# Optimization experiments

Measured on AMD Instinct MI355X. Metric: run time of the kernel, lower is better.

The kernel has to match this reference:

```python
import jax, jax.numpy as jnp
import numpy as np
import math

B, TQ, TK, D = 4, 1024, 1024, 1024
H, DK, DV = 16, 64, 64


def _ln(x, g, b, eps=1e-5):
    m = x.mean(-1, keepdims=True)
    v = ((x - m) ** 2).mean(-1, keepdims=True)
    return (x - m) * jax.lax.rsqrt(v + eps) * g + b


def setup_inputs() -> dict:
    key = jax.random.key(0)
    ks = jax.random.split(key, 24)
    s = 0.02
    inp = {
        "x": jax.random.normal(ks[0], (B, TQ, D), jnp.float32),
        "y": jax.random.normal(ks[1], (B, TK, D), jnp.float32),
        "mask": jax.random.randint(ks[2], (B, TK), 0, 2).astype(bool),
        # pre-attention layernorms (affine)
        "ln1_g": jnp.ones((D,)), "ln1_b": jnp.zeros((D,)),
        "ln2_g": jnp.ones((D,)), "ln2_b": jnp.zeros((D,)),
        # mha1 projections
        "q_w": jax.random.normal(ks[3], (D, H * DK)) * s, "q_b": jnp.zeros((H * DK,)),
        "k_w": jax.random.normal(ks[4], (D, H * DK)) * s, "k_b": jnp.zeros((H * DK,)),
        "v_w": jax.random.normal(ks[5], (D, H * DV)) * s, "v_b": jnp.zeros((H * DV,)),
        "o_w": jax.random.normal(ks[6], (H * DV, D)) * s, "o_b": jnp.zeros((D,)),
        # MLP: [LN, ReLU, Linear] x 2 over sizes [D, D, D]
        "mln1_g": jnp.ones((D,)), "mln1_b": jnp.zeros((D,)),
        "l1_w": jax.random.normal(ks[7], (D, D)) * s, "l1_b": jnp.zeros((D,)),
        "mln2_g": jnp.ones((D,)), "mln2_b": jnp.zeros((D,)),
        "l2_w": jax.random.normal(ks[8], (D, D)) * s, "l2_b": jnp.zeros((D,)),
    }
    return inp


def reference(x, y, mask, ln1_g, ln1_b, ln2_g, ln2_b,
              q_w, q_b, k_w, k_b, v_w, v_b, o_w, o_b,
              mln1_g, mln1_b, l1_w, l1_b, mln2_g, mln2_b, l2_w, l2_b):
    # pre-norm + relu
    x1 = jax.nn.relu(_ln(x, ln1_g, ln1_b))
    y1 = jax.nn.relu(_ln(y, ln2_g, ln2_b))
    # cross attention (mha1)
    b, t, _ = x1.shape
    q = (x1 @ q_w + q_b).reshape(b, t, H, DK)
    k = (y1 @ k_w + k_b).reshape(b, -1, H, DK)
    v = (y1 @ v_w + v_b).reshape(b, -1, H, DV)
    logits = jnp.einsum('bthd,bThd->bhtT', q, k) * (1.0 / math.sqrt(DK))
    logits = jnp.where(mask[:, None, None, :], logits, -1e30)
    w = jax.nn.softmax(logits, axis=-1)
    attn = jnp.einsum('bhtT,bThd->bthd', w, v).reshape(b, t, H * DV)
    x = x + (attn @ o_w + o_b)
    # MLP: LN -> ReLU -> Linear, twice
    h = jax.nn.relu(_ln(x, mln1_g, mln1_b)) @ l1_w + l1_b
    out = jax.nn.relu(_ln(h, mln2_g, mln2_b)) @ l2_w + l2_b
    return out
```

## Files before the change

### kernel.cpp

```cpp
#include <hip/hip_runtime.h>
#include <hip/hip_bf16.h>
#include <math.h>

#define D_MODEL 1024
#define NTOK    4096

typedef unsigned short u16;
typedef unsigned int   u32;
typedef __attribute__((ext_vector_type(8))) short  short8;
typedef __attribute__((ext_vector_type(4))) float  floatx4;
typedef __attribute__((ext_vector_type(4))) unsigned short ushort4v;
typedef __attribute__((ext_vector_type(2))) unsigned int   uint2v;

static __host__ __device__ __forceinline__ float bf2f(u16 u) {
    union { unsigned int i; float f; } v; v.i = ((unsigned int)u) << 16; return v.f;
}
static __host__ __device__ __forceinline__ u16 f2bf(float f) {
    union { float f; unsigned int i; } v; v.f = f;
    unsigned int r = (v.i + 0x7FFFu + ((v.i >> 16) & 1u)) >> 16;
    return (u16)r;
}
static __device__ __forceinline__ u32 fbits(float f) {
    union { float f; u32 i; } v; v.f = f; return v.i;
}
static __device__ __forceinline__ float fexp2(float x) {
    float r; asm("v_exp_f32 %0, %1" : "=v"(r) : "v"(x)); return r;
}
static __device__ __forceinline__ void gl2lds16(const void* g, void* l) {
    __builtin_amdgcn_global_load_lds(
        (const __attribute__((address_space(1))) void*)g,
        (__attribute__((address_space(3))) void*)l, 16, 0, 0);
}

__global__ __launch_bounds__(256) void CrossTransformer_27522150432886_kernel(
    float* __restrict__ out, int n, float val)
{
    int i = blockIdx.x * 256 + threadIdx.x;
    if (i < n) out[i] = val;
}

struct PreArgs {
    const float* w[6]; u16* wt;
    const float* x; const float* g1; const float* b1; u16* xn;
    const float* y; const float* g2; const float* b2; u16* yn;
    const void* maskp; float* madd;
};
__global__ __launch_bounds__(256) void pre_k(PreArgs a)
{
    __shared__ __align__(16) char shm[2176];
    const int blk = blockIdx.x, t = threadIdx.x;

    if (blk < 6144) {
        u16 (*tile)[33] = (u16(*)[33])shm;
        const int wz = blk >> 10, tl = blk & 1023;
        const int c0 = (tl & 31) * 32, r0 = (tl >> 5) * 32;
        const int tx = t & 31, ty = t >> 5;
        const float* W  = a.w[wz];
        u16*         Wt = a.wt + (size_t)wz * D_MODEL * D_MODEL;
#pragma unroll
        for (int j = 0; j < 4; j++)
            tile[ty + j * 8][tx] = f2bf(W[(size_t)(r0 + ty + j * 8) * D_MODEL + c0 + tx]);
        __syncthreads();
#pragma unroll
        for (int j = 0; j < 4; j++)
            Wt[(size_t)(c0 + ty + j * 8) * D_MODEL + r0 + tx] = tile[tx][ty + j * 8];
        return;
    }
    if (blk < 14336) {
        const int isY = blk >= 10240;
        const int row = blk - (isY ? 10240 : 6144);
        const float* in  = isY ? a.y  : a.x;
        const float* gam = isY ? a.g2 : a.g1;
        const float* bet = isY ? a.b2 : a.b1;
        u16*         out = isY ? a.yn : a.xn;
        float (*red)[4] = (float(*)[4])shm;

        const float4 p = *(const float4*)(in + (size_t)row * D_MODEL + t * 4);
        float v0 = p.x, v1 = p.y, v2 = p.z, v3 = p.w;
        float s = v0 + v1 + v2 + v3;
        float q = v0 * v0 + v1 * v1 + v2 * v2 + v3 * v3;
#pragma unroll
        for (int off = 32; off > 0; off >>= 1) {
            s += __shfl_xor(s, off, 64);
            q += __shfl_xor(q, off, 64);
        }
        if ((t & 63) == 0) { red[0][t >> 6] = s; red[1][t >> 6] = q; }
        __syncthreads();
        s = red[0][0] + red[0][1] + red[0][2] + red[0][3];
        q = red[1][0] + red[1][1] + red[1][2] + red[1][3];
        const float mean = s * (1.0f / D_MODEL);
        const float var  = q * (1.0f / D_MODEL) - mean * mean;
        const float rstd = rsqrtf(var + 1e-5f);
        const float4 gp = *(const float4*)(gam + t * 4);
        const float4 bp = *(const float4*)(bet + t * 4);
        ushort4v o;
        o[0] = f2bf(fmaxf((v0 - mean) * rstd * gp.x + bp.x, 0.f));
        o[1] = f2bf(fmaxf((v1 - mean) * rstd * gp.y + bp.y, 0.f));
        o[2] = f2bf(fmaxf((v2 - mean) * rstd * gp.z + bp.z, 0.f));
        o[3] = f2bf(fmaxf((v3 - mean) * rstd * gp.w + bp.w, 0.f));
        *(ushort4v*)(out + (size_t)row * D_MODEL + t * 4) = o;
        return;
    }
    {
        int* rb = (int*)shm;
        const unsigned int* wv = (const unsigned int*)a.maskp;
        int bad = 0;
        for (int i = t; i < 1024; i += 256) {
            unsigned int v = wv[i];
            if (!(v == 0u || v == 1u || v == 0xFFu || v == 0xFFFFFFFFu)) bad++;
        }
#pragma unroll
        for (int off = 32; off > 0; off >>= 1) bad += __shfl_xor(bad, off, 64);
        if ((t & 63) == 0) rb[t >> 6] = bad;
        __syncthreads();
        const int Bc = rb[0] + rb[1] + rb[2] + rb[3];
        if (Bc * 2 > 1024) {
            const unsigned char* b8 = (const unsigned char*)a.maskp;
            for (int i = t; i < 4096; i += 256) a.madd[i] = b8[i] ? 0.f : -1e30f;
        } else {
            const int* m32 = (const int*)a.maskp;
            for (int i = t; i < 4096; i += 256) a.madd[i] = m32[i] ? 0.f : -1e30f;
        }
    }
}

__global__ __launch_bounds__(256) void ln_relu_k(
    const void* __restrict__ in, const float* __restrict__ gam,
    const float* __restrict__ bet, u16* __restrict__ out)
{
    const int row = blockIdx.x, t = threadIdx.x;
    ushort4v u = *(const ushort4v*)((const u16*)in + (size_t)row * D_MODEL + t * 4);
    float v0 = bf2f(u[0]), v1 = bf2f(u[1]), v2 = bf2f(u[2]), v3 = bf2f(u[3]);
    float s = v0 + v1 + v2 + v3;
    float q = v0 * v0 + v1 * v1 + v2 * v2 + v3 * v3;
#pragma unroll
    for (int off = 32; off > 0; off >>= 1) {
        s += __shfl_xor(s, off, 64);
        q += __shfl_xor(q, off, 64);
    }
    __shared__ float red[2][4];
    if ((t & 63) == 0) { red[0][t >> 6] = s; red[1][t >> 6] = q; }
    __syncthreads();
    s = red[0][0] + red[0][1] + red[0][2] + red[0][3];
    q = red[1][0] + red[1][1] + red[1][2] + red[1][3];

    const float mean = s * (1.0f / D_MODEL);
    const float var  = q * (1.0f / D_MODEL) - mean * mean;
    const float rstd = rsqrtf(var + 1e-5f);

    const float4 gp = *(const float4*)(gam + t * 4);
    const float4 bp = *(const float4*)(bet + t * 4);
    ushort4v o;
    o[0] = f2bf(fmaxf((v0 - mean) * rstd * gp.x + bp.x, 0.f));
    o[1] = f2bf(fmaxf((v1 - mean) * rstd * gp.y + bp.y, 0.f));
    o[2] = f2bf(fmaxf((v2 - mean) * rstd * gp.z + bp.z, 0.f));
    o[3] = f2bf(fmaxf((v3 - mean) * rstd * gp.w + bp.w, 0.f));
    *(ushort4v*)(out + (size_t)row * D_MODEL + t * 4) = o;
}

struct GB {
    const u16* A; const u16* Bt; const float* bias; const float* resid;
    u16* C; float* Cf; float scale; int vt;
};
struct GB3 { GB g[3]; u16* VtG; };

__global__ __launch_bounds__(512) void gemm_qkv256_k(GB3 gb)
{
    extern __shared__ char smc[];
    const int lin = blockIdx.x;
    const int t8  = (lin & 7) * 24 + (lin >> 3);
    const int z   = t8 >> 6;
    const int rem = t8 & 63;
    const GB cfg = gb.g[z];
    const int t = threadIdx.x, lane = t & 63, w = t >> 6;
    const int wy = w >> 2, wx = w & 3;
    const int bm = (rem >> 2) * 256, bn = (rem & 3) * 256;
    const int m = lane & 15, g = lane >> 4;
    const int srcseg = ((t & 3) ^ ((t >> 3) & 3)) * 8;
    const int gsw    = (g ^ ((m >> 1) & 3)) * 8;

    const u16* Ag = cfg.A  + (size_t)(bm + (t >> 2)) * D_MODEL + srcseg;
    const u16* Bg = cfg.Bt + (size_t)(bn + (t >> 2)) * D_MODEL + srcseg;

    auto stage_half = [&](int kt, int s, int buf) {
        const int koff = kt + s * 32;
        char* base = smc + buf * 65536 + s * 32768;
        gl2lds16(Ag + koff,                 base + t * 16);
        gl2lds16(Ag + 128 * D_MODEL + koff, base + 8192 + t * 16);
        gl2lds16(Bg + koff,                 base + 16384 + t * 16);
        gl2lds16(Bg + 128 * D_MODEL + koff, base + 24576 + t * 16);
    };

    floatx4 acc[8][4] = {};
    const int NT = D_MODEL / 64;

    stage_half(0, 0, 0);
    stage_half(0, 1, 0);

    int buf = 0;
    for (int tt = 0; tt < NT; ++tt) {
        const int ktn = ((tt + 1) & (NT - 1)) * 64;
        const int nbuf = buf ^ 1;
#pragma unroll
        for (int s = 0; s < 2; ++s) {
            asm volatile("s_waitcnt vmcnt(4)" ::: "memory");
            __builtin_amdgcn_s_barrier();
            stage_half(ktn, s, nbuf);

            const u16* As = (const u16*)(smc + buf * 65536 + s * 32768);
            const u16* Bs = As + 8192;
            short8 af[8], bf[4];
#pragma unroll
            for (int mt = 0; mt < 8; mt++)
                af[mt] = *(const short8*)(As + (wy * 128 + mt * 16 + m) * 32 + gsw);
#pragma unroll
            for (int nt = 0; nt < 4; nt++)
                bf[nt] = *(const short8*)(Bs + (wx * 64 + nt * 16 + m) * 32 + gsw);

            __builtin_amdgcn_s_setprio(1);
#pragma unroll
            for (int mt = 0; mt < 8; mt++)
#pragma unroll
                for (int nt = 0; nt < 4; nt++)
                    acc[mt][nt] = __builtin_amdgcn_mfma_f32_16x16x32_bf16(
                        af[mt], bf[nt], acc[mt][nt], 0, 0, 0);
            __builtin_amdgcn_s_setprio(0);
        }
        buf ^= 1;
    }
    asm volatile("s_waitcnt vmcnt(0)" ::: "memory");
    __builtin_amdgcn_s_barrier();

    float bv[4];
#pragma unroll
    for (int nt = 0; nt < 4; nt++)
        bv[nt] = cfg.bias[bn + wx * 64 + nt * 16 + m];

    if (!cfg.vt) {
#pragma unroll
        for (int mt = 0; mt < 8; mt++)
#pragma unroll
            for (int r = 0; r < 4; r++) {
                const int grow = bm + wy * 128 + mt * 16 + g * 4 + r;
#pragma unroll
                for (int nt = 0; nt < 4; nt++) {
                    const int col = bn + wx * 64 + nt * 16 + m;
                    float val = (acc[mt][nt][r] + bv[nt]) * cfg.scale;
                    cfg.C[(size_t)grow * D_MODEL + col] = f2bf(val);
                }
            }
    } else {
        const int b    = bm >> 10;
        const int tok0 = bm & 1023;
#pragma unroll
        for (int mt = 0; mt < 8; mt++) {
            const int tok = tok0 + wy * 128 + mt * 16 + g * 4;
#pragma unroll
            for (int nt = 0; nt < 4; nt++) {
                const int col = bn + wx * 64 + nt * 16 + m;
                const int h = col >> 6, d = col & 63;
                ushort4v o;
                o[0] = f2bf(acc[mt][nt][0] + bv[nt]);
                o[1] = f2bf(acc[mt][nt][1] + bv[nt]);
                o[2] = f2bf(acc[mt][nt][2] + bv[nt]);
                o[3] = f2bf(acc[mt][nt][3] + bv[nt]);
                *(ushort4v*)(gb.VtG + ((size_t)((b * 16 + h) * 64 + d)) * 1024 + tok) = o;
            }
        }
    }
}

__global__ __launch_bounds__(512) void gemm_out_k(GB cfg)
{
    const int lin = blockIdx.x + 8 * blockIdx.y;
    const int t8  = (lin & 7) * 32 + (lin >> 3);
    __shared__ __align__(16) u16 sm[3 * 8192];
    const int t = threadIdx.x, lane = t & 63, w = t >> 6;
    const int wy = w >> 2, wx = w & 3;
    const int bm = (t8 >> 3) * 128, bn = (t8 & 7) * 128;
    const int m = lane & 15, g = lane >> 4;
    const int arow = t >> 2;
    const int aseg = ((t & 3) ^ ((t >> 3) & 3)) * 8;
    const int gsw  = (g ^ ((m >> 1) & 3)) * 8;

    const u16* Ag = cfg.A  + (size_t)(bm + arow) * D_MODEL + aseg;
    const u16* Bg = cfg.Bt + (size_t)(bn + arow) * D_MODEL + aseg;

    auto stage = [&](int k0, int s) {
        char* dst = (char*)sm + s * 16384;
        gl2lds16(Ag + k0, dst + w * 1024);
        gl2lds16(Bg + k0, dst + 8192 + w * 1024);
    };

    floatx4 acc[4][2] = {};
    const int NT = D_MODEL / 32;

    stage(0, 0);
    stage(32, 1);
    asm volatile("s_waitcnt vmcnt(2)" ::: "memory");
    __builtin_amdgcn_s_barrier();

    int sb = 0;
    for (int tt = 0; tt < NT; ++tt) {
        int tp = tt + 2; if (tp >= NT) tp -= NT;
        int sbp = sb + 2; if (sbp >= 3) sbp -= 3;
        stage(tp * 32, sbp);

        const u16* As = sm + sb * 8192;
        const u16* Bs = As + 4096;
        short8 af[4], bf[2];
#pragma unroll
        for (int mt = 0; mt < 4; mt++)
            af[mt] = *(const short8*)(As + (wy * 64 + mt * 16 + m) * 32 + gsw);
#pragma unroll
        for (int nt = 0; nt < 2; nt++)
            bf[nt] = *(const short8*)(Bs + (wx * 32 + nt * 16 + m) * 32 + gsw);

        __builtin_amdgcn_s_setprio(1);
#pragma unroll
        for (int mt = 0; mt < 4; mt++)
#pragma unroll
            for (int nt = 0; nt < 2; nt++)
                acc[mt][nt] = __builtin_amdgcn_mfma_f32_16x16x32_bf16(
                    af[mt], bf[nt], acc[mt][nt], 0, 0, 0);
        __builtin_amdgcn_s_setprio(0);

        asm volatile("s_waitcnt vmcnt(2)" ::: "memory");
        __builtin_amdgcn_s_barrier();
        sb = sb + 1; if (sb >= 3) sb -= 3;
    }
    asm volatile("s_waitcnt vmcnt(0)" ::: "memory");

    float bv[2]; int cols[2];
#pragma unroll
    for (int nt = 0; nt < 2; nt++) {
        cols[nt] = bn + wx * 32 + nt * 16 + m;
        bv[nt]   = cfg.bias[cols[nt]];
    }
#pragma unroll
    for (int mt = 0; mt < 4; mt++) {
#pragma unroll
        for (int r = 0; r < 4; r++) {
            const int grow = bm + wy * 64 + mt * 16 + g * 4 + r;
#pragma unroll
            for (int nt = 0; nt < 2; nt++) {
                float val = acc[mt][nt][r] + bv[nt];
                if (cfg.resid) val += cfg.resid[(size_t)grow * D_MODEL + cols[nt]];
                if (cfg.Cf) cfg.Cf[(size_t)grow * D_MODEL + cols[nt]] = val;
                else        cfg.C [(size_t)grow * D_MODEL + cols[nt]] = f2bf(val);
            }
        }
    }
}

__global__ __launch_bounds__(256) void attn_k(
    const u16* __restrict__ Q, const u16* __restrict__ Kk,
    const u16* __restrict__ VtG, const float* __restrict__ maddG,
    u16* __restrict__ Ob)
{
    __shared__ __align__(16) char smraw[55808];
    u16*   KsB  = (u16*)smraw;
    u16*   VtB  = (u16*)(smraw + 16384);
    u16*   Ps   = (u16*)(smraw + 32768);
    float* madd = (float*)(smraw + 51200);
    float* liS  = (float*)(smraw + 55296);

    const int lin = blockIdx.x + 8 * (blockIdx.y + 16 * blockIdx.z);
    const int tw  = (lin & 7) * 64 + (lin >> 3);
    const int qt = tw & 7, h = (tw >> 3) & 15, b = tw >> 7;
    const int t = threadIdx.x, lane = t & 63, w = t >> 6;
    const int m = lane & 15, g = lane >> 4;

    for (int i = t; i < 1024; i += 256) madd[i] = maddG[b * 1024 + i];

    short8 qf[2][2];
    const u16* Qb = Q + ((size_t)(b * 1024 + qt * 128 + w * 32 + m)) * D_MODEL + h * 64 + g * 8;
#pragma unroll
    for (int q2 = 0; q2 < 2; q2++)
#pragma unroll
        for (int hf = 0; hf < 2; hf++)
            qf[q2][hf] = *(const short8*)(Qb + q2 * 16 * D_MODEL + hf * 32);

    u16* Pw = Ps + w * 32 * 72;
    const u16* Kp = Kk  + (size_t)(b * 1024) * D_MODEL + h * 64;
    const u16* Vp = VtG + (size_t)((b * 16 + h) * 64) * 1024;

    const int r0 = lane >> 3;
    const int ssl = ((lane & 7) ^ r0) * 8;
    auto stageKV = [&](int kt, int bufI) {
#pragma unroll
        for (int i = 0; i < 2; i++) {
            const int row = w * 16 + i * 8 + r0;
            gl2lds16(Kp + (size_t)(kt + row) * D_MODEL + ssl,
                     (char*)(KsB + bufI * 4096) + (w * 2 + i) * 1024);
            gl2lds16(Vp + (size_t)row * 1024 + kt + ssl,
                     (char*)(VtB + bufI * 4096) + (w * 2 + i) * 1024);
        }
    };

    floatx4 Ov[2][4] = {};
    float li[2] = { 0.f, 0.f };

    const int s8  = m & 7;
    const int sl0 = (g ^ s8) * 8;
    const int sl1 = sl0 ^ 32;

    stageKV(0, 0);
    __syncthreads();

    int buf = 0;
    for (int kt = 0; kt < 1024; kt += 64) {
        if (kt + 64 < 1024) stageKV(kt + 64, buf ^ 1);

        const u16* Ks = KsB + buf * 4096;
        const u16* Vt = VtB + buf * 4096;

        short8 af[4][2];
        float4 md[4];
#pragma unroll
        for (int tile = 0; tile < 4; tile++) {
            af[tile][0] = *(const short8*)(Ks + (tile * 16 + m) * 64 + sl0);
            af[tile][1] = *(const short8*)(Ks + (tile * 16 + m) * 64 + sl1);
            md[tile]    = *(const float4*)(madd + kt + tile * 16 + g * 4);
        }

#pragma unroll
        for (int q2 = 0; q2 < 2; q2++) {
            floatx4 st[4];
            __builtin_amdgcn_s_setprio(1);
#pragma unroll
            for (int tile = 0; tile < 4; tile++) {
                floatx4 z = {};
                z = __builtin_amdgcn_mfma_f32_16x16x32_bf16(af[tile][0], qf[q2][0], z, 0, 0, 0);
                st[tile] = __builtin_amdgcn_mfma_f32_16x16x32_bf16(af[tile][1], qf[q2][1], z, 0, 0, 0);
            }
            __builtin_amdgcn_s_setprio(0);
            float rs = 0.f;
#pragma unroll
            for (int tile = 0; tile < 4; tile++) {
                float p0 = fexp2(st[tile][0] + md[tile].x);
                float p1 = fexp2(st[tile][1] + md[tile].y);
                float p2 = fexp2(st[tile][2] + md[tile].z);
                float p3 = fexp2(st[tile][3] + md[tile].w);
                rs += (p0 + p1) + (p2 + p3);
                uint2v pk;
                pk[0] = __builtin_amdgcn_perm(fbits(p1), fbits(p0), 0x07060302u);
                pk[1] = __builtin_amdgcn_perm(fbits(p3), fbits(p2), 0x07060302u);
                *(uint2v*)(Pw + (q2 * 16 + m) * 72 + tile * 16 + g * 4) = pk;
            }
            rs += __shfl_xor(rs, 16, 64);
            rs += __shfl_xor(rs, 32, 64);
            li[q2] += rs;
        }

        short8 pa[2][2], vb[4][2];
#pragma unroll
        for (int q2 = 0; q2 < 2; q2++) {
            pa[q2][0] = *(const short8*)(Pw + (q2 * 16 + m) * 72 + g * 8);
            pa[q2][1] = *(const short8*)(Pw + (q2 * 16 + m) * 72 + 32 + g * 8);
        }
#pragma unroll
        for (int nt = 0; nt < 4; nt++) {
            vb[nt][0] = *(const short8*)(Vt + (nt * 16 + m) * 64 + sl0);
            vb[nt][1] = *(const short8*)(Vt + (nt * 16 + m) * 64 + sl1);
        }
        __builtin_amdgcn_s_setprio(1);
#pragma unroll
        for (int q2 = 0; q2 < 2; q2++)
#pragma unroll
            for (int nt = 0; nt < 4; nt++) {
                Ov[q2][nt] = __builtin_amdgcn_mfma_f32_16x16x32_bf16(
                    pa[q2][0], vb[nt][0], Ov[q2][nt], 0, 0, 0);
                Ov[q2][nt] = __builtin_amdgcn_mfma_f32_16x16x32_bf16(
                    pa[q2][1], vb[nt][1], Ov[q2][nt], 0, 0, 0);
            }
        __builtin_amdgcn_s_setprio(0);

        asm volatile("s_waitcnt vmcnt(0)" ::: "memory");
        __builtin_amdgcn_s_barrier();
        buf ^= 1;
    }

    if (g == 0) { liS[w * 32 + m] = li[0]; liS[w * 32 + 16 + m] = li[1]; }
    __builtin_amdgcn_s_waitcnt(0);
    float4 inv4[2];
#pragma unroll
    for (int q2 = 0; q2 < 2; q2++) {
        float4 l4 = *(const float4*)(liS + w * 32 + q2 * 16 + g * 4);
        inv4[q2].x = 1.0f / fmaxf(l4.x, 1e-37f);
        inv4[q2].y = 1.0f / fmaxf(l4.y, 1e-37f);
        inv4[q2].z = 1.0f / fmaxf(l4.z, 1e-37f);
        inv4[q2].w = 1.0f / fmaxf(l4.w, 1e-37f);
    }
#pragma unroll
    for (int q2 = 0; q2 < 2; q2++) {
        const float iv[4] = { inv4[q2].x, inv4[q2].y, inv4[q2].z, inv4[q2].w };
#pragma unroll
        for (int nt = 0; nt < 4; nt++)
#pragma unroll
            for (int r = 0; r < 4; r++) {
                const int tok = qt * 128 + w * 32 + q2 * 16 + g * 4 + r;
                Ob[(size_t)(b * 1024 + tok) * D_MODEL + h * 64 + nt * 16 + m] =
                    f2bf(Ov[q2][nt][r] * iv[r]);
            }
    }
}

extern "C" __attribute__((visibility("default")))
void kernel_launch(void* const* d_in, const int* in_sizes, int n_in,
                   void* d_out, int out_size, void* d_ws, size_t ws_size,
                   hipStream_t stream)
{
    (void)in_sizes; (void)n_in;
    const float* x      = (const float*)d_in[0];
    const float* y      = (const float*)d_in[1];
    const void*  maskp  = d_in[2];
    const float* ln1_g  = (const float*)d_in[3];
    const float* ln1_b  = (const float*)d_in[4];
    const float* ln2_g  = (const float*)d_in[5];
    const float* ln2_b  = (const float*)d_in[6];
    const float* q_w    = (const float*)d_in[7];
    const float* q_b    = (const float*)d_in[8];
    const float* k_w    = (const float*)d_in[9];
    const float* k_b    = (const float*)d_in[10];
    const float* v_w    = (const float*)d_in[11];
    const float* v_b    = (const float*)d_in[12];
    const float* o_w    = (const float*)d_in[13];
    const float* o_b    = (const float*)d_in[14];
    const float* mln1_g = (const float*)d_in[15];
    const float* mln1_b = (const float*)d_in[16];
    const float* l1_w   = (const float*)d_in[17];
    const float* l1_b   = (const float*)d_in[18];
    const float* mln2_g = (const float*)d_in[19];
    const float* mln2_b = (const float*)d_in[20];
    const float* l2_w   = (const float*)d_in[21];
    const float* l2_b   = (const float*)d_in[22];

    const int nout = out_size;
    const size_t MB = 1024 * 1024;
    if (ws_size < 61 * MB) {
        CrossTransformer_27522150432886_kernel<<<(nout + 255) / 256, 256, 0, stream>>>(
            (float*)d_out, nout, 7.0f);
        return;
    }

    static bool attrSet = false;
    if (!attrSet) {
        hipFuncSetAttribute((const void*)gemm_qkv256_k,
                            hipFuncAttributeMaxDynamicSharedMemorySize, 131072);
        attrSet = true;
    }

    char* ws = (char*)d_ws;
    const size_t WE = (size_t)D_MODEL * D_MODEL;
    u16*   wt   = (u16*)(ws);
    u16*   xn   = (u16*)(ws + 12 * MB);
    u16*   yn   = (u16*)(ws + 20 * MB);
    u16*   Qb   = (u16*)(ws + 28 * MB);
    u16*   Kb   = (u16*)(ws + 36 * MB);
    u16*   VtG  = (u16*)(ws + 44 * MB);
    u16*   attn = (u16*)(ws + 52 * MB);
    float* madd = (float*)(ws + 60 * MB);
    u16* x2 = xn; u16* m1n = Qb; u16* hb = Kb; u16* m2n = VtG;

    PreArgs pa;
    pa.w[0] = q_w; pa.w[1] = k_w; pa.w[2] = v_w;
    pa.w[3] = o_w; pa.w[4] = l1_w; pa.w[5] = l2_w;
    pa.wt = wt;
    pa.x = x; pa.g1 = ln1_g; pa.b1 = ln1_b; pa.xn = xn;
    pa.y = y; pa.g2 = ln2_g; pa.b2 = ln2_b; pa.yn = yn;
    pa.maskp = maskp; pa.madd = madd;
    pre_k<<<14337, 256, 0, stream>>>(pa);

    const float qscale = 0.18033688011112042f;
    GB3 qkv = {};
    qkv.g[0] = GB{ xn, wt + 0 * WE, q_b, nullptr, Qb, nullptr, qscale, 0 };
    qkv.g[1] = GB{ yn, wt + 1 * WE, k_b, nullptr, Kb, nullptr, 1.0f,  0 };
    qkv.g[2] = GB{ yn, wt + 2 * WE, v_b, nullptr, nullptr, nullptr, 1.0f, 1 };
    qkv.VtG = VtG;
    gemm_qkv256_k<<<192, 512, 131072, stream>>>(qkv);

    attn_k<<<dim3(8, 16, 4), 256, 0, stream>>>(Qb, Kb, VtG, madd, attn);

    GB go = GB{ attn, wt + 3 * WE, o_b, x, x2, nullptr, 1.0f, 0 };
    gemm_out_k<<<dim3(8, 32, 1), 512, 0, stream>>>(go);

    ln_relu_k<<<NTOK, 256, 0, stream>>>(x2, mln1_g, mln1_b, m1n);

    GB g1 = GB{ m1n, wt + 4 * WE, l1_b, nullptr, hb, nullptr, 1.0f, 0 };
    gemm_out_k<<<dim3(8, 32, 1), 512, 0, stream>>>(g1);

    ln_relu_k<<<NTOK, 256, 0, stream>>>(hb, mln2_g, mln2_b, m2n);

    GB g2 = GB{ m2n, wt + 5 * WE, l2_b, nullptr, nullptr, (float*)d_out, 1.0f, 0 };
    gemm_out_k<<<dim3(8, 32, 1), 512, 0, stream>>>(g2);
}
```

Measured before the change: 270.0 us.

## Split-K the post-attention GEMMs and fuse reduction with bias, residual and LayerNorm

The three 4096x1024x1024 GEMMs after attention are now split along K into two halves, using 256-thread blocks with 128x128 tiles over 512 blocks, and write fp32 partials to the workspace. A row-wise kernel then sums the two partials and adds bias and residual, and for the first two GEMMs also applies the following LayerNorm+ReLU. This removes the separate ln_relu passes and bf16 rounding of intermediates, and aims for better CU occupancy. The cost is extra fp32 partial traffic (32MB written and read per GEMM) and a larger workspace requirement.

New measurement: 282.5 us. +4.6%, slower.

```diff
diff --git a/kernel.cpp b/kernel.cpp
--- a/kernel.cpp
+++ b/kernel.cpp
@@ -124,40 +124,6 @@
     }
 }
 
-__global__ __launch_bounds__(256) void ln_relu_k(
-    const void* __restrict__ in, const float* __restrict__ gam,
-    const float* __restrict__ bet, u16* __restrict__ out)
-{
-    const int row = blockIdx.x, t = threadIdx.x;
-    ushort4v u = *(const ushort4v*)((const u16*)in + (size_t)row * D_MODEL + t * 4);
-    float v0 = bf2f(u[0]), v1 = bf2f(u[1]), v2 = bf2f(u[2]), v3 = bf2f(u[3]);
-    float s = v0 + v1 + v2 + v3;
-    float q = v0 * v0 + v1 * v1 + v2 * v2 + v3 * v3;
-#pragma unroll
-    for (int off = 32; off > 0; off >>= 1) {
-        s += __shfl_xor(s, off, 64);
-        q += __shfl_xor(q, off, 64);
-    }
-    __shared__ float red[2][4];
-    if ((t & 63) == 0) { red[0][t >> 6] = s; red[1][t >> 6] = q; }
-    __syncthreads();
-    s = red[0][0] + red[0][1] + red[0][2] + red[0][3];
-    q = red[1][0] + red[1][1] + red[1][2] + red[1][3];
-
-    const float mean = s * (1.0f / D_MODEL);
-    const float var  = q * (1.0f / D_MODEL) - mean * mean;
-    const float rstd = rsqrtf(var + 1e-5f);
-
-    const float4 gp = *(const float4*)(gam + t * 4);
-    const float4 bp = *(const float4*)(bet + t * 4);
-    ushort4v o;
-    o[0] = f2bf(fmaxf((v0 - mean) * rstd * gp.x + bp.x, 0.f));
-    o[1] = f2bf(fmaxf((v1 - mean) * rstd * gp.y + bp.y, 0.f));
-    o[2] = f2bf(fmaxf((v2 - mean) * rstd * gp.z + bp.z, 0.f));
-    o[3] = f2bf(fmaxf((v3 - mean) * rstd * gp.w + bp.w, 0.f));
-    *(ushort4v*)(out + (size_t)row * D_MODEL + t * 4) = o;
-}
-
 struct GB {
     const u16* A; const u16* Bt; const float* bias; const float* resid;
     u16* C; float* Cf; float scale; int vt;
@@ -270,34 +236,41 @@
     }
 }
 
-__global__ __launch_bounds__(512) void gemm_out_k(GB cfg)
-{
-    const int lin = blockIdx.x + 8 * blockIdx.y;
-    const int t8  = (lin & 7) * 32 + (lin >> 3);
+__global__ __launch_bounds__(256) void gemm_ks_k(
+    const u16* __restrict__ A, const u16* __restrict__ Bt, float* __restrict__ P)
+{
+    const int lin = blockIdx.x;
+    const int t8  = (lin & 7) * 64 + (lin >> 3);
+    const int ks  = t8 >> 8;
+    const int rem = t8 & 255;
     __shared__ __align__(16) u16 sm[3 * 8192];
     const int t = threadIdx.x, lane = t & 63, w = t >> 6;
-    const int wy = w >> 2, wx = w & 3;
-    const int bm = (t8 >> 3) * 128, bn = (t8 & 7) * 128;
+    const int wy = w >> 1, wx = w & 1;
+    const int bm = (rem >> 3) * 128, bn = (rem & 7) * 128;
     const int m = lane & 15, g = lane >> 4;
     const int arow = t >> 2;
     const int aseg = ((t & 3) ^ ((t >> 3) & 3)) * 8;
     const int gsw  = (g ^ ((m >> 1) & 3)) * 8;
-
-    const u16* Ag = cfg.A  + (size_t)(bm + arow) * D_MODEL + aseg;
-    const u16* Bg = cfg.Bt + (size_t)(bn + arow) * D_MODEL + aseg;
+    const int kb   = ks * 512;
+
+    const u16* Ag = A  + (size_t)(bm + arow) * D_MODEL + kb + aseg;
+    const u16* Bg = Bt + (size_t)(bn + arow) * D_MODEL + kb + aseg;
 
     auto stage = [&](int k0, int s) {
         char* dst = (char*)sm + s * 16384;
-        gl2lds16(Ag + k0, dst + w * 1024);
-        gl2lds16(Bg + k0, dst + 8192 + w * 1024);
+#pragma unroll
+        for (int i = 0; i < 2; i++) {
+            gl2lds16(Ag + (size_t)(i * 64) * D_MODEL + k0, dst + i * 4096 + w * 1024);
+            gl2lds16(Bg + (size_t)(i * 64) * D_MODEL + k0, dst + 8192 + i * 4096 + w * 1024);
+        }
     };
 
-    floatx4 acc[4][2] = {};
-    const int NT = D_MODEL / 32;
+    floatx4 acc[4][4] = {};
+    const int NT = 16;
 
     stage(0, 0);
     stage(32, 1);
-    asm volatile("s_waitcnt vmcnt(2)" ::: "memory");
+    asm volatile("s_waitcnt vmcnt(4)" ::: "memory");
     __builtin_amdgcn_s_barrier();
 
     int sb = 0;
@@ -308,49 +281,97 @@
 
         const u16* As = sm + sb * 8192;
         const u16* Bs = As + 4096;
-        short8 af[4], bf[2];
+        short8 af[4], bf[4];
 #pragma unroll
         for (int mt = 0; mt < 4; mt++)
             af[mt] = *(const short8*)(As + (wy * 64 + mt * 16 + m) * 32 + gsw);
 #pragma unroll
-        for (int nt = 0; nt < 2; nt++)
-            bf[nt] = *(const short8*)(Bs + (wx * 32 + nt * 16 + m) * 32 + gsw);
+        for (int nt = 0; nt < 4; nt++)
+            bf[nt] = *(const short8*)(Bs + (wx * 64 + nt * 16 + m) * 32 + gsw);
 
         __builtin_amdgcn_s_setprio(1);
 #pragma unroll
         for (int mt = 0; mt < 4; mt++)
 #pragma unroll
-            for (int nt = 0; nt < 2; nt++)
+            for (int nt = 0; nt < 4; nt++)
                 acc[mt][nt] = __builtin_amdgcn_mfma_f32_16x16x32_bf16(
                     af[mt], bf[nt], acc[mt][nt], 0, 0, 0);
         __builtin_amdgcn_s_setprio(0);
 
-        asm volatile("s_waitcnt vmcnt(2)" ::: "memory");
+        asm volatile("s_waitcnt vmcnt(4)" ::: "memory");
         __builtin_amdgcn_s_barrier();
         sb = sb + 1; if (sb >= 3) sb -= 3;
     }
     asm volatile("s_waitcnt vmcnt(0)" ::: "memory");
 
-    float bv[2]; int cols[2];
-#pragma unroll
-    for (int nt = 0; nt < 2; nt++) {
-        cols[nt] = bn + wx * 32 + nt * 16 + m;
-        bv[nt]   = cfg.bias[cols[nt]];
-    }
-#pragma unroll
-    for (int mt = 0; mt < 4; mt++) {
+    float* Pk = P + (size_t)ks * NTOK * D_MODEL;
+#pragma unroll
+    for (int mt = 0; mt < 4; mt++)
 #pragma unroll
         for (int r = 0; r < 4; r++) {
             const int grow = bm + wy * 64 + mt * 16 + g * 4 + r;
 #pragma unroll
-            for (int nt = 0; nt < 2; nt++) {
-                float val = acc[mt][nt][r] + bv[nt];
-                if (cfg.resid) val += cfg.resid[(size_t)grow * D_MODEL + cols[nt]];
-                if (cfg.Cf) cfg.Cf[(size_t)grow * D_MODEL + cols[nt]] = val;
-                else        cfg.C [(size_t)grow * D_MODEL + cols[nt]] = f2bf(val);
+            for (int nt = 0; nt < 4; nt++) {
+                const int col = bn + wx * 64 + nt * 16 + m;
+                Pk[(size_t)grow * D_MODEL + col] = acc[mt][nt][r];
             }
         }
-    }
+}
+
+__global__ __launch_bounds__(256) void lnred_k(
+    const float* __restrict__ P, const float* __restrict__ bias,
+    const float* __restrict__ resid, const float* __restrict__ gam,
+    const float* __restrict__ bet, u16* __restrict__ out)
+{
+    const int row = blockIdx.x, t = threadIdx.x;
+    const size_t off = (size_t)row * D_MODEL + t * 4;
+    const float4 p0 = *(const float4*)(P + off);
+    const float4 p1 = *(const float4*)(P + (size_t)NTOK * D_MODEL + off);
+    const float4 bb = *(const float4*)(bias + t * 4);
+    float v0 = p0.x + p1.x + bb.x, v1 = p0.y + p1.y + bb.y;
+    float v2 = p0.z + p1.z + bb.z, v3 = p0.w + p1.w + bb.w;
+    if (resid) {
+        const float4 rr = *(const float4*)(resid + off);
+        v0 += rr.x; v1 += rr.y; v2 += rr.z; v3 += rr.w;
+    }
+    float s = v0 + v1 + v2 + v3;
+    float q = v0 * v0 + v1 * v1 + v2 * v2 + v3 * v3;
+#pragma unroll
+    for (int o = 32; o > 0; o >>= 1) {
+        s += __shfl_xor(s, o, 64);
+        q += __shfl_xor(q, o, 64);
+    }
+    __shared__ float red[2][4];
+    if ((t & 63) == 0) { red[0][t >> 6] = s; red[1][t >> 6] = q; }
+    __syncthreads();
+    s = red[0][0] + red[0][1] + red[0][2] + red[0][3];
+    q = red[1][0] + red[1][1] + red[1][2] + red[1][3];
+    const float mean = s * (1.0f / D_MODEL);
+    const float var  = q * (1.0f / D_MODEL) - mean * mean;
+    const float rstd = rsqrtf(var + 1e-5f);
+    const float4 gp = *(const float4*)(gam + t * 4);
+    const float4 bp = *(const float4*)(bet + t * 4);
+    ushort4v o;
+    o[0] = f2bf(fmaxf((v0 - mean) * rstd * gp.x + bp.x, 0.f));
+    o[1] = f2bf(fmaxf((v1 - mean) * rstd * gp.y + bp.y, 0.f));
+    o[2] = f2bf(fmaxf((v2 - mean) * rstd * gp.z + bp.z, 0.f));
+    o[3] = f2bf(fmaxf((v3 - mean) * rstd * gp.w + bp.w, 0.f));
+    *(ushort4v*)(out + (size_t)row * D_MODEL + t * 4) = o;
+}
+
+__global__ __launch_bounds__(256) void redout_k(
+    const float* __restrict__ P, const float* __restrict__ bias,
+    float* __restrict__ out)
+{
+    const int row = blockIdx.x, t = threadIdx.x;
+    const size_t off = (size_t)row * D_MODEL + t * 4;
+    const float4 p0 = *(const float4*)(P + off);
+    const float4 p1 = *(const float4*)(P + (size_t)NTOK * D_MODEL + off);
+    const float4 bb = *(const float4*)(bias + t * 4);
+    float4 o;
+    o.x = p0.x + p1.x + bb.x; o.y = p0.y + p1.y + bb.y;
+    o.z = p0.z + p1.z + bb.z; o.w = p0.w + p1.w + bb.w;
+    *(float4*)(out + off) = o;
 }
 
 __global__ __launch_bounds__(256) void attn_k(
@@ -538,7 +559,7 @@
 
     const int nout = out_size;
     const size_t MB = 1024 * 1024;
-    if (ws_size < 61 * MB) {
+    if (ws_size < 97 * MB) {
         CrossTransformer_27522150432886_kernel<<<(nout + 255) / 256, 256, 0, stream>>>(
             (float*)d_out, nout, 7.0f);
         return;
@@ -561,7 +582,8 @@
     u16*   VtG  = (u16*)(ws + 44 * MB);
     u16*   attn = (u16*)(ws + 52 * MB);
     float* madd = (float*)(ws + 60 * MB);
-    u16* x2 = xn; u16* m1n = Qb; u16* hb = Kb; u16* m2n = VtG;
+    float* Pp   = (float*)(ws + 64 * MB);
+    u16* m1n = Qb; u16* m2n = VtG;
 
     PreArgs pa;
     pa.w[0] = q_w; pa.w[1] = k_w; pa.w[2] = v_w;
@@ -582,16 +604,12 @@
 
     attn_k<<<dim3(8, 16, 4), 256, 0, stream>>>(Qb, Kb, VtG, madd, attn);
 
-    GB go = GB{ attn, wt + 3 * WE, o_b, x, x2, nullptr, 1.0f, 0 };
-    gemm_out_k<<<dim3(8, 32, 1), 512, 0, stream>>>(go);
-
-    ln_relu_k<<<NTOK, 256, 0, stream>>>(x2, mln1_g, mln1_b, m1n);
-
-    GB g1 = GB{ m1n, wt + 4 * WE, l1_b, nullptr, hb, nullptr, 1.0f, 0 };
-    gemm_out_k<<<dim3(8, 32, 1), 512, 0, stream>>>(g1);
-
-    ln_relu_k<<<NTOK, 256, 0, stream>>>(hb, mln2_g, mln2_b, m2n);
-
-    GB g2 = GB{ m2n, wt + 5 * WE, l2_b, nullptr, nullptr, (float*)d_out, 1.0f, 0 };
-    gemm_out_k<<<dim3(8, 32, 1), 512, 0, stream>>>(g2);
-}
+    gemm_ks_k<<<512, 256, 0, stream>>>(attn, wt + 3 * WE, Pp);
+    lnred_k<<<NTOK, 256, 0, stream>>>(Pp, o_b, x, mln1_g, mln1_b, m1n);
+
+    gemm_ks_k<<<512, 256, 0, stream>>>(m1n, wt + 4 * WE, Pp);
+    lnred_k<<<NTOK, 256, 0, stream>>>(Pp, l1_b, nullptr, mln2_g, mln2_b, m2n);
+
+    gemm_ks_k<<<512, 256, 0, stream>>>(m2n, wt + 5 * WE, Pp);
+    redout_k<<<NTOK, 256, 0, stream>>>(Pp, l2_b, (float*)d_out);
+}
```
